# Kernel optimization log

Hardware: AMD Instinct MI355X
Metric: run time of the kernel (lower is better)

Reference implementation:

```python
import jax, jax.numpy as jnp
import numpy as np

N = 40000   # num nodes
C = 128     # in_channels
H = 8       # num_heads
D = C // H  # head_dim = 16
E = 640000  # num edges
FF = 4 * C


def layer_norm(x, g, b, eps=1e-5):
    m = jnp.mean(x, axis=-1, keepdims=True)
    v = jnp.mean((x - m) ** 2, axis=-1, keepdims=True)
    return (x - m) / jnp.sqrt(v + eps) * g + b


def setup_inputs() -> dict:
    key = jax.random.key(0)
    ks = jax.random.split(key, 16)
    s = 0.02
    x = jax.random.normal(ks[0], (N, C), dtype=jnp.float32)
    edge_index = jax.random.randint(ks[1], (2, E), 0, N, dtype=jnp.int64)
    return {
        'x': x,
        'edge_index': edge_index,
        'Wq': jax.random.normal(ks[2], (C, C), jnp.float32) * s,
        'bq': jnp.zeros((C,), jnp.float32),
        'Wk': jax.random.normal(ks[3], (C, C), jnp.float32) * s,
        'bk': jnp.zeros((C,), jnp.float32),
        'Wv': jax.random.normal(ks[4], (C, C), jnp.float32) * s,
        'bv': jnp.zeros((C,), jnp.float32),
        'Wo': jax.random.normal(ks[5], (C, C), jnp.float32) * s,
        'bo': jnp.zeros((C,), jnp.float32),
        'ln1_g': jnp.ones((C,), jnp.float32),
        'ln1_b': jnp.zeros((C,), jnp.float32),
        'ln2_g': jnp.ones((C,), jnp.float32),
        'ln2_b': jnp.zeros((C,), jnp.float32),
        'W1': jax.random.normal(ks[6], (C, FF), jnp.float32) * s,
        'b1': jnp.zeros((FF,), jnp.float32),
        'W2': jax.random.normal(ks[7], (FF, C), jnp.float32) * s,
        'b2': jnp.zeros((C,), jnp.float32),
    }


def reference(x, edge_index, Wq, bq, Wk, bk, Wv, bv, Wo, bo,
              ln1_g, ln1_b, ln2_g, ln2_b, W1, b1, W2, b2):
    residual = x
    xn = layer_norm(x, ln1_g, ln1_b)
    q = (xn @ Wq + bq).reshape(N, H, D)
    k = (xn @ Wk + bk).reshape(N, H, D)
    v = (xn @ Wv + bv).reshape(N, H, D)
    src, dst = edge_index[0], edge_index[1]
    # per-edge scores: [E, H]
    scores = jnp.einsum('ehd,ehd->eh', q[dst], k[src]) / jnp.sqrt(jnp.float32(D))
    # NOTE: faithful to the source — softmax over ALL edges (dim=0), not per-destination
    attn = jax.nn.softmax(scores, axis=0)[:, :, None]          # [E, H, 1]
    weighted = v[src] * attn                                   # [E, H, D]
    aggregated = jax.ops.segment_sum(weighted, dst, num_segments=N)  # [N, H, D]
    out = aggregated.reshape(N, C) @ Wo + bo
    x1 = residual + out
    residual2 = x1
    xn2 = layer_norm(x1, ln2_g, ln2_b)
    ffn = jax.nn.relu(xn2 @ W1 + b1) @ W2 + b2
    return residual2 + ffn
```

## Files before the change

kernel.cpp:

```cpp
#include <hip/hip_runtime.h>
#include <math.h>

#define NNODES 40000
#define CCH    128
#define NH     8
#define HD     16
#define NEDGE  640000
#define NBLK   157
#define FBLK   10000
#define RBLK   40

typedef __attribute__((ext_vector_type(8))) short bf16x8;
typedef __attribute__((ext_vector_type(4))) float f32x4;
typedef __attribute__((ext_vector_type(2))) float f32x2;

__device__ inline unsigned short f2bf(float f) {
  union { float f; unsigned u; } c; c.f = f;
  unsigned r = c.u + 0x7fffu + ((c.u >> 16) & 1u);
  return (unsigned short)(r >> 16);
}
__device__ inline float bfs(unsigned short u) { union { unsigned i; float f; } c; c.i = (unsigned)u << 16; return c.f; }
__device__ inline float bflo(unsigned u) { union { unsigned i; float f; } c; c.i = u << 16; return c.f; }
__device__ inline float bfhi(unsigned u) { union { unsigned i; float f; } c; c.i = u & 0xffff0000u; return c.f; }

__device__ inline unsigned char f2fp8(float v) {
#if __has_builtin(__builtin_amdgcn_cvt_pk_fp8_f32)
  return (unsigned char)(__builtin_amdgcn_cvt_pk_fp8_f32(v, v, 0, false) & 0xff);
#else
  union { float f; unsigned u; } c; c.f = v;
  unsigned s = (c.u >> 24) & 0x80;
  int e = (int)((c.u >> 23) & 0xff) - 127;
  unsigned m = c.u & 0x7fffff;
  if (e > 8) return s | 0x7e;
  if (e >= -6) {
    unsigned q = (m + 0x80000) >> 20; unsigned ee = e + 7;
    if (q == 8) { q = 0; ee++; }
    if (ee > 15) return s | 0x7e;
    return s | (ee << 3) | q;
  }
  if (e < -10) return (unsigned char)s;
  float a = fabsf(v); unsigned q = (unsigned)(a * 512.f + 0.5f); if (q > 7) q = 7;
  return s | q;
#endif
}
__device__ inline void fp8x4d(unsigned w, float* o) {
#if __has_builtin(__builtin_amdgcn_cvt_pk_f32_fp8)
  f32x2 lo = __builtin_amdgcn_cvt_pk_f32_fp8((int)w, false);
  f32x2 hi = __builtin_amdgcn_cvt_pk_f32_fp8((int)w, true);
  o[0] = lo[0]; o[1] = lo[1]; o[2] = hi[0]; o[3] = hi[1];
#else
  #pragma unroll
  for (int i = 0; i < 4; i++) {
    unsigned b = (w >> (8 * i)) & 0xff;
    unsigned s = b >> 7, e = (b >> 3) & 15, m = b & 7;
    float v;
    if (e) { union { unsigned u; float f; } c; c.u = ((e + 120) << 23) | (m << 20); v = c.f; }
    else v = m * (1.f / 512.f);
    o[i] = s ? -v : v;
  }
#endif
}

__global__ __launch_bounds__(256) void k_ln_bf(const float* __restrict__ x,
                                               const float* __restrict__ g,
                                               const float* __restrict__ b,
                                               unsigned* __restrict__ out) {
  int wave = threadIdx.x >> 6;
  int lane = threadIdx.x & 63;
  int row  = blockIdx.x * 4 + wave;
  if (row >= NNODES) return;
  const float2* xr = (const float2*)(x + (size_t)row * CCH);
  float2 v = xr[lane];
  float s  = v.x + v.y;
  float ss = v.x * v.x + v.y * v.y;
  #pragma unroll
  for (int d = 1; d < 64; d <<= 1) {
    s  += __shfl_xor(s, d);
    ss += __shfl_xor(ss, d);
  }
  float mean = s * (1.0f / CCH);
  float var  = ss * (1.0f / CCH) - mean * mean;
  float rstd = rsqrtf(var + 1e-5f);
  float2 gg = ((const float2*)g)[lane];
  float2 bb = ((const float2*)b)[lane];
  float ox = (v.x - mean) * rstd * gg.x + bb.x;
  float oy = (v.y - mean) * rstd * gg.y + bb.y;
  out[(size_t)row * 64 + lane] = ((unsigned)f2bf(oy) << 16) | f2bf(ox);
}

__global__ __launch_bounds__(256) void k_wprep_all(const float* __restrict__ Wq,
                                                   const float* __restrict__ Wk,
                                                   const float* __restrict__ Wv,
                                                   const float* __restrict__ W1,
                                                   const float* __restrict__ W2,
                                                   const float* __restrict__ bq,
                                                   const float* __restrict__ bk,
                                                   const float* __restrict__ bv,
                                                   unsigned short* __restrict__ Wqkvt,
                                                   unsigned short* __restrict__ W1t,
                                                   unsigned short* __restrict__ W2t,
                                                   float* __restrict__ bqkv) {
  int idx = blockIdx.x * 256 + threadIdx.x;
  if (idx < 16384) { int n = idx >> 7, k = idx & 127; Wqkvt[idx] = f2bf(Wq[(size_t)k * 128 + n]); return; }
  idx -= 16384;
  if (idx < 16384) { int n = idx >> 7, k = idx & 127; Wqkvt[16384 + (n << 7) + k] = f2bf(Wk[(size_t)k * 128 + n]); return; }
  idx -= 16384;
  if (idx < 16384) { int n = idx >> 7, k = idx & 127; Wqkvt[32768 + (n << 7) + k] = f2bf(Wv[(size_t)k * 128 + n]); return; }
  idx -= 16384;
  if (idx < 65536) { int n = idx >> 7, k = idx & 127; W1t[idx] = f2bf(W1[(size_t)k * 512 + n]); return; }
  idx -= 65536;
  if (idx < 65536) { int n = idx >> 9, k = idx & 511; W2t[idx] = f2bf(W2[(size_t)k * 128 + n]); return; }
  idx -= 65536;
  if (idx < 384) bqkv[idx] = idx < 128 ? bq[idx] : (idx < 256 ? bk[idx - 128] : bv[idx - 256]);
}

__global__ __launch_bounds__(256) void k_wprep_wo(const float* __restrict__ W,
                                                  const float* __restrict__ dpart,
                                                  unsigned short* __restrict__ Wt) {
  __shared__ float sinv[8];
  if (threadIdx.x < 64) {
    int h = threadIdx.x & 7;
    float s = 0.f;
    for (int r = threadIdx.x >> 3; r < RBLK; r += 8) s += dpart[r * 8 + h];
    #pragma unroll
    for (int d = 8; d < 64; d <<= 1) s += __shfl_xor(s, d);
    if (threadIdx.x < 8) sinv[h] = 1.0f / s;
  }
  __syncthreads();
  int idx = blockIdx.x * 256 + threadIdx.x;
  if (idx >= CCH * CCH) return;
  int n = idx >> 7, k = idx & 127;
  Wt[idx] = f2bf(W[(size_t)k * CCH + n] * sinv[k >> 4]);
}

template <bool RELU, int RESMODE, int MODE>
__global__ __launch_bounds__(256) void k_mgemm(const unsigned short* __restrict__ A,
                                               const unsigned short* __restrict__ Bt,
                                               const float* __restrict__ bias,
                                               const void* __restrict__ res,
                                               void* __restrict__ outp,
                                               int K, int Nc,
                                               const float* __restrict__ lng,
                                               const float* __restrict__ lnb,
                                               void* __restrict__ outp2) {
  __shared__ unsigned short As[64 * 64];
  __shared__ unsigned short Bs[128 * 64];
  const int tid  = threadIdx.x;
  const int row0 = blockIdx.x * 64;
  const int c0   = blockIdx.y * 128;
  const int l    = tid & 63;
  const int w    = tid >> 6;
  const int wr   = w >> 1;
  const int wc   = w & 1;

  f32x4 acc[2][4] = {};

  for (int kc = 0; kc < K; kc += 64) {
    __syncthreads();
    #pragma unroll
    for (int it = 0; it < 2; it++) {
      int idx = it * 256 + tid;
      int r = idx >> 3, s = idx & 7;
      uint4 vv = *(const uint4*)(A + (size_t)(row0 + r) * K + kc + s * 8);
      *(uint4*)(As + r * 64 + ((s ^ (r & 7)) * 8)) = vv;
    }
    #pragma unroll
    for (int it = 0; it < 4; it++) {
      int idx = it * 256 + tid;
      int n = idx >> 3, s = idx & 7;
      uint4 vv = *(const uint4*)(Bt + (size_t)(c0 + n) * K + kc + s * 8);
      *(uint4*)(Bs + n * 64 + ((s ^ (n & 7)) * 8)) = vv;
    }
    __syncthreads();
    #pragma unroll
    for (int kk = 0; kk < 2; kk++) {
      int sb = kk * 4 + (l >> 4);
      bf16x8 af[2], bfr[4];
      #pragma unroll
      for (int mi = 0; mi < 2; mi++) {
        int r = wr * 32 + mi * 16 + (l & 15);
        af[mi] = *(const bf16x8*)(As + r * 64 + ((sb ^ (r & 7)) * 8));
      }
      #pragma unroll
      for (int ni = 0; ni < 4; ni++) {
        int n = wc * 64 + ni * 16 + (l & 15);
        bfr[ni] = *(const bf16x8*)(Bs + n * 64 + ((sb ^ (n & 7)) * 8));
      }
      #pragma unroll
      for (int mi = 0; mi < 2; mi++)
        #pragma unroll
        for (int ni = 0; ni < 4; ni++)
          acc[mi][ni] = __builtin_amdgcn_mfma_f32_16x16x32_bf16(af[mi], bfr[ni], acc[mi][ni], 0, 0, 0);
    }
  }

  if constexpr (MODE == 3) {
    __shared__ float lnS[64][2], lnSS[64][2], gS[128], bS[128];
    if (tid < 128) { gS[tid] = lng[tid]; bS[tid] = lnb[tid]; }
    #pragma unroll
    for (int mi = 0; mi < 2; mi++) {
      #pragma unroll
      for (int p = 0; p < 4; p++) {
        int lr = wr * 32 + mi * 16 + (l >> 4) * 4 + p;
        int r  = row0 + lr;
        float s = 0.f, ss = 0.f;
        #pragma unroll
        for (int ni = 0; ni < 4; ni++) {
          int c = wc * 64 + ni * 16 + (l & 15);
          float val = acc[mi][ni][p] + bias[c] + ((const float*)res)[(size_t)r * 128 + c];
          acc[mi][ni][p] = val;
          s += val; ss += val * val;
        }
        #pragma unroll
        for (int d = 1; d < 16; d <<= 1) { s += __shfl_xor(s, d); ss += __shfl_xor(ss, d); }
        if ((l & 15) == 0) { lnS[lr][wc] = s; lnSS[lr][wc] = ss; }
      }
    }
    __syncthreads();
    #pragma unroll
    for (int mi = 0; mi < 2; mi++) {
      #pragma unroll
      for (int p = 0; p < 4; p++) {
        int lr = wr * 32 + mi * 16 + (l >> 4) * 4 + p;
        int r  = row0 + lr;
        float m   = (lnS[lr][0] + lnS[lr][1]) * (1.f / 128.f);
        float var = (lnSS[lr][0] + lnSS[lr][1]) * (1.f / 128.f) - m * m;
        float rstd = rsqrtf(var + 1e-5f);
        #pragma unroll
        for (int ni = 0; ni < 4; ni++) {
          int c = wc * 64 + ni * 16 + (l & 15);
          float val = acc[mi][ni][p];
          ((unsigned short*)outp)[(size_t)r * 128 + c]  = f2bf(val);
          ((unsigned short*)outp2)[(size_t)r * 128 + c] = f2bf((val - m) * rstd * gS[c] + bS[c]);
        }
      }
    }
  } else {
    #pragma unroll
    for (int mi = 0; mi < 2; mi++) {
      #pragma unroll
      for (int p = 0; p < 4; p++) {
        int r = row0 + wr * 32 + mi * 16 + (l >> 4) * 4 + p;
        #pragma unroll
        for (int ni = 0; ni < 4; ni++) {
          int c = c0 + wc * 64 + ni * 16 + (l & 15);
          float val = acc[mi][ni][p] + bias[c];
          if (RESMODE == 1) val += ((const float*)res)[(size_t)r * Nc + c];
          if (RESMODE == 2) val += bfs(((const unsigned short*)res)[(size_t)r * Nc + c]);
          if (RELU) val = fmaxf(val, 0.f);
          if (MODE == 0)      ((float*)outp)[(size_t)r * Nc + c] = val;
          else if (MODE == 1) ((unsigned short*)outp)[(size_t)r * Nc + c] = f2bf(val);
          else {
            char* rowb = (char*)outp + (size_t)r * 512;
            if (c < 128) *(unsigned short*)(rowb + c * 2) = f2bf(val);
            else         *(unsigned char*)(rowb + 256 + (c - 128)) = f2fp8(val);
          }
        }
      }
    }
  }
}

__global__ __launch_bounds__(256) void k_histrank(const int* __restrict__ ei,
                                                  int* __restrict__ deg,
                                                  int* __restrict__ rank) {
  int e = blockIdx.x * 256 + threadIdx.x;
  if (e >= NEDGE) return;
  rank[e] = atomicAdd(&deg[ei[NEDGE + e]], 1);
}

__global__ __launch_bounds__(256) void k_scan3a(const int* __restrict__ deg,
                                                int* __restrict__ bsum) {
  int i = blockIdx.x * 256 + threadIdx.x;
  int d = (i < NNODES) ? deg[i] : 0;
  #pragma unroll
  for (int s = 1; s < 64; s <<= 1) d += __shfl_xor(d, s);
  __shared__ int ws4[4];
  if ((threadIdx.x & 63) == 0) ws4[threadIdx.x >> 6] = d;
  __syncthreads();
  if (threadIdx.x == 0) bsum[blockIdx.x] = ws4[0] + ws4[1] + ws4[2] + ws4[3];
}

__global__ __launch_bounds__(256) void k_scan3b(const int* __restrict__ bsum,
                                                int* __restrict__ bpre) {
  int t = threadIdx.x;
  int d = (t < NBLK) ? bsum[t] : 0;
  int lane = t & 63, wv = t >> 6;
  int incl = d;
  #pragma unroll
  for (int s = 1; s < 64; s <<= 1) { int o = __shfl_up(incl, s); if (lane >= s) incl += o; }
  __shared__ int wsum[4];
  if (lane == 63) wsum[wv] = incl;
  __syncthreads();
  int base = 0;
  for (int w2 = 0; w2 < wv; w2++) base += wsum[w2];
  if (t < NBLK) bpre[t] = base + incl - d;
}

__global__ __launch_bounds__(256) void k_scan3c(const int* __restrict__ deg,
                                                const int* __restrict__ bpre,
                                                int* __restrict__ off) {
  int t = threadIdx.x;
  int i = blockIdx.x * 256 + t;
  int d = (i < NNODES) ? deg[i] : 0;
  int lane = t & 63, wv = t >> 6;
  int incl = d;
  #pragma unroll
  for (int s = 1; s < 64; s <<= 1) { int o = __shfl_up(incl, s); if (lane >= s) incl += o; }
  __shared__ int wsum[4];
  if (lane == 63) wsum[wv] = incl;
  __syncthreads();
  int base = bpre[blockIdx.x];
  for (int w2 = 0; w2 < wv; w2++) base += wsum[w2];
  int ex = base + incl - d;
  if (i < NNODES) off[i] = ex;
  if (i == 0) off[NNODES] = NEDGE;
}

__global__ __launch_bounds__(256) void k_scatter(const int* __restrict__ ei,
                                                 const int* __restrict__ off,
                                                 const int* __restrict__ rank,
                                                 int* __restrict__ srcs) {
  int e = blockIdx.x * 256 + threadIdx.x;
  if (e >= NEDGE) return;
  srcs[off[ei[NEDGE + e]] + rank[e]] = ei[e];
}

__global__ __launch_bounds__(256) void k_fused(const unsigned char* __restrict__ qkv,
                                               const int* __restrict__ off,
                                               const int* __restrict__ srcs,
                                               unsigned* __restrict__ U,
                                               float* __restrict__ hpart) {
  const int wave = threadIdx.x >> 6;
  const int lane = threadIdx.x & 63;
  const int n  = blockIdx.x * 4 + wave;
  const int g  = lane >> 3;
  const int c8 = lane & 7;

  const uint4* qp = (const uint4*)(qkv + (size_t)n * 512 + c8 * 32);
  uint4 qa = qp[0], qb = qp[1];
  float qf[16];
  qf[0]=bflo(qa.x);  qf[1]=bfhi(qa.x);  qf[2]=bflo(qa.y);  qf[3]=bfhi(qa.y);
  qf[4]=bflo(qa.z);  qf[5]=bfhi(qa.z);  qf[6]=bflo(qa.w);  qf[7]=bfhi(qa.w);
  qf[8]=bflo(qb.x);  qf[9]=bfhi(qb.x);  qf[10]=bflo(qb.y); qf[11]=bfhi(qb.y);
  qf[12]=bflo(qb.z); qf[13]=bfhi(qb.z); qf[14]=bflo(qb.w); qf[15]=bfhi(qb.w);

  float acc[16];
  #pragma unroll
  for (int i = 0; i < 16; i++) acc[i] = 0.f;
  float lsum = 0.f;

  const int i0 = off[n], i1 = off[n + 1];
  for (int jb = i0; jb < i1; jb += 8) {
    int j = jb + g;
    bool valid = j < i1;
    int src = srcs[valid ? j : jb];
    const uint4* kp = (const uint4*)(qkv + (size_t)src * 512 + 256 + c8 * 16);
    uint4 kw = kp[0];
    uint4 vw = kp[8];
    float kf[16], vf[16];
    fp8x4d(kw.x, kf + 0); fp8x4d(kw.y, kf + 4); fp8x4d(kw.z, kf + 8); fp8x4d(kw.w, kf + 12);
    fp8x4d(vw.x, vf + 0); fp8x4d(vw.y, vf + 4); fp8x4d(vw.z, vf + 8); fp8x4d(vw.w, vf + 12);
    float p = 0.f;
    #pragma unroll
    for (int i = 0; i < 16; i++) p += qf[i] * kf[i];
    float w = valid ? __expf(p * 0.25f) : 0.f;
    lsum += w;
    #pragma unroll
    for (int i = 0; i < 16; i++) acc[i] += w * vf[i];
  }

  #pragma unroll
  for (int d = 8; d < 64; d <<= 1) {
    #pragma unroll
    for (int i = 0; i < 16; i++) acc[i] += __shfl_xor(acc[i], d);
    lsum += __shfl_xor(lsum, d);
  }

  __shared__ float wsum[4][8];
  if (lane < 8) {
    wsum[wave][c8] = lsum;
    unsigned o[8];
    #pragma unroll
    for (int i = 0; i < 8; i++)
      o[i] = ((unsigned)f2bf(acc[2 * i + 1]) << 16) | f2bf(acc[2 * i]);
    uint4* up = (uint4*)(U + (size_t)n * 64 + c8 * 8);
    up[0] = make_uint4(o[0], o[1], o[2], o[3]);
    up[1] = make_uint4(o[4], o[5], o[6], o[7]);
  }
  __syncthreads();
  if (threadIdx.x < 8) {
    hpart[blockIdx.x * 8 + threadIdx.x] =
        wsum[0][threadIdx.x] + wsum[1][threadIdx.x] + wsum[2][threadIdx.x] + wsum[3][threadIdx.x];
  }
}

__global__ __launch_bounds__(256) void k_reduce_part(const float* __restrict__ hpart,
                                                     float* __restrict__ dpart) {
  const int t = threadIdx.x;
  const int h = t & 7;
  const int r0 = blockIdx.x * (FBLK / RBLK);
  float s = 0.f;
  for (int r = r0 + (t >> 3); r < r0 + FBLK / RBLK; r += 32) s += hpart[r * 8 + h];
  #pragma unroll
  for (int d = 8; d < 64; d <<= 1) s += __shfl_xor(s, d);
  __shared__ float ws4[4][8];
  int lane = t & 63, wv = t >> 6;
  if (lane < 8) ws4[wv][lane] = s;
  __syncthreads();
  if (t < 8) dpart[blockIdx.x * 8 + t] = ws4[0][t] + ws4[1][t] + ws4[2][t] + ws4[3][t];
}

extern "C" void kernel_launch(void* const* d_in, const int* in_sizes, int n_in,
                              void* d_out, int out_size, void* d_ws, size_t ws_size,
                              hipStream_t stream) {
  const float* x    = (const float*)d_in[0];
  const int*   ei   = (const int*)d_in[1];
  const float* Wq   = (const float*)d_in[2];
  const float* bq   = (const float*)d_in[3];
  const float* Wk   = (const float*)d_in[4];
  const float* bk   = (const float*)d_in[5];
  const float* Wv   = (const float*)d_in[6];
  const float* bv   = (const float*)d_in[7];
  const float* Wo   = (const float*)d_in[8];
  const float* bo   = (const float*)d_in[9];
  const float* ln1g = (const float*)d_in[10];
  const float* ln1b = (const float*)d_in[11];
  const float* ln2g = (const float*)d_in[12];
  const float* ln2b = (const float*)d_in[13];
  const float* W1   = (const float*)d_in[14];
  const float* b1   = (const float*)d_in[15];
  const float* W2   = (const float*)d_in[16];
  const float* b2   = (const float*)d_in[17];
  float* out = (float*)d_out;

  char* p = (char*)d_ws;
  const size_t NCb = (size_t)NNODES * CCH * 2;
  unsigned short* xn   = (unsigned short*)p; p += NCb;
  unsigned char*  qkvb = (unsigned char*)p;  p += (size_t)NNODES * 512;
  unsigned short* agg  = (unsigned short*)p; p += NCb;
  p += NCb;
  unsigned short* x1b  = (unsigned short*)p; p += NCb;
  int* deg    = (int*)p;                     p += (size_t)NNODES * 4 + 256;
  int* off    = (int*)p;                     p += (size_t)(NNODES + 1) * 4 + 256;
  int* rank   = (int*)p;                     p += (size_t)NEDGE * 4;
  int* srcs   = (int*)p;                     p += (size_t)NEDGE * 4;
  int* bsum   = (int*)p;                     p += 256 * 4;
  int* bpre   = (int*)p;                     p += 256 * 4;
  float* hpart = (float*)p;                  p += (size_t)FBLK * 8 * 4;
  float* dpart = (float*)p;                  p += (size_t)RBLK * 8 * 4 + 256;
  float* bqkv  = (float*)p;                  p += 384 * 4 + 256;
  unsigned short* Wqkvt = (unsigned short*)p; p += (size_t)384 * CCH * 2;
  unsigned short* Wot   = (unsigned short*)p; p += (size_t)CCH * CCH * 2;
  unsigned short* W1t   = (unsigned short*)p; p += (size_t)CCH * 4 * CCH * 2;
  unsigned short* W2t   = (unsigned short*)p; p += (size_t)CCH * 4 * CCH * 2;
  unsigned short* ffn1 = (unsigned short*)qkvb;
  unsigned short* xn2  = xn;

  dim3 blk(256);
  dim3 gLN(NNODES / 4);
  dim3 gM(NNODES / 64, 1);
  dim3 gM3(NNODES / 64, 3);
  dim3 gM4(NNODES / 64, 4);
  dim3 gE((NEDGE + 255) / 256);

  hipMemsetAsync(deg, 0, (size_t)NNODES * 4, stream);
  k_histrank<<<gE, blk, 0, stream>>>(ei, deg, rank);
  k_scan3a<<<NBLK, blk, 0, stream>>>(deg, bsum);
  k_scan3b<<<1, blk, 0, stream>>>(bsum, bpre);
  k_scan3c<<<NBLK, blk, 0, stream>>>(deg, bpre, off);
  k_scatter<<<gE, blk, 0, stream>>>(ei, off, rank, srcs);

  k_wprep_all<<<706, blk, 0, stream>>>(Wq, Wk, Wv, W1, W2, bq, bk, bv,
                                       Wqkvt, W1t, W2t, bqkv);

  k_ln_bf<<<gLN, blk, 0, stream>>>(x, ln1g, ln1b, (unsigned*)xn);
  k_mgemm<false, 0, 2><<<gM3, blk, 0, stream>>>(xn, Wqkvt, bqkv, nullptr, qkvb,
                                                CCH, 384, nullptr, nullptr, nullptr);

  k_fused<<<FBLK, blk, 0, stream>>>(qkvb, off, srcs, (unsigned*)agg, hpart);
  k_reduce_part<<<RBLK, blk, 0, stream>>>(hpart, dpart);

  k_wprep_wo<<<64, blk, 0, stream>>>(Wo, dpart, Wot);
  k_mgemm<false, 1, 3><<<gM, blk, 0, stream>>>(agg, Wot, bo, x, x1b,
                                               CCH, CCH, ln2g, ln2b, xn2);

  k_mgemm<true, 0, 1><<<gM4, blk, 0, stream>>>(xn2, W1t, b1, nullptr, ffn1,
                                               CCH, 4 * CCH, nullptr, nullptr, nullptr);
  k_mgemm<false, 2, 0><<<gM, blk, 0, stream>>>(ffn1, W2t, b2, x1b, out,
                                               4 * CCH, CCH, nullptr, nullptr, nullptr);
}
```

Measured before the change: 167.5 us.

## Fuse LayerNorm into QKV GEMM, add K=128 GEMM kernel, prefetch edges

Adds a specialized K=128 GEMM kernel that keeps the whole A tile in LDS and loops over all output column tiles in one block. The QKV projection now computes LayerNorm inline from fp32 x, which removes the separate LN kernel and its bf16 round trip. The FFN1 GEMM uses the same kernel, so A is loaded once rather than once per column block. The deg memset is folded into the weight-prep kernel, and the edge-aggregation loop now prefetches the next batch of K/V before using the current one. The cost is less grid parallelism (one block per 64 rows) and larger LDS use per block.

Result: faster. 161.4 us (-3.6%).

```diff
diff --git a/kernel.cpp b/kernel.cpp
--- a/kernel.cpp
+++ b/kernel.cpp
@@ -61,33 +61,6 @@
 #endif
 }
 
-__global__ __launch_bounds__(256) void k_ln_bf(const float* __restrict__ x,
-                                               const float* __restrict__ g,
-                                               const float* __restrict__ b,
-                                               unsigned* __restrict__ out) {
-  int wave = threadIdx.x >> 6;
-  int lane = threadIdx.x & 63;
-  int row  = blockIdx.x * 4 + wave;
-  if (row >= NNODES) return;
-  const float2* xr = (const float2*)(x + (size_t)row * CCH);
-  float2 v = xr[lane];
-  float s  = v.x + v.y;
-  float ss = v.x * v.x + v.y * v.y;
-  #pragma unroll
-  for (int d = 1; d < 64; d <<= 1) {
-    s  += __shfl_xor(s, d);
-    ss += __shfl_xor(ss, d);
-  }
-  float mean = s * (1.0f / CCH);
-  float var  = ss * (1.0f / CCH) - mean * mean;
-  float rstd = rsqrtf(var + 1e-5f);
-  float2 gg = ((const float2*)g)[lane];
-  float2 bb = ((const float2*)b)[lane];
-  float ox = (v.x - mean) * rstd * gg.x + bb.x;
-  float oy = (v.y - mean) * rstd * gg.y + bb.y;
-  out[(size_t)row * 64 + lane] = ((unsigned)f2bf(oy) << 16) | f2bf(ox);
-}
-
 __global__ __launch_bounds__(256) void k_wprep_all(const float* __restrict__ Wq,
                                                    const float* __restrict__ Wk,
                                                    const float* __restrict__ Wv,
@@ -99,8 +72,11 @@
                                                    unsigned short* __restrict__ Wqkvt,
                                                    unsigned short* __restrict__ W1t,
                                                    unsigned short* __restrict__ W2t,
-                                                   float* __restrict__ bqkv) {
-  int idx = blockIdx.x * 256 + threadIdx.x;
+                                                   float* __restrict__ bqkv,
+                                                   int* __restrict__ deg) {
+  int g0 = blockIdx.x * 256 + threadIdx.x;
+  if (g0 < NNODES) deg[g0] = 0;
+  int idx = g0;
   if (idx < 16384) { int n = idx >> 7, k = idx & 127; Wqkvt[idx] = f2bf(Wq[(size_t)k * 128 + n]); return; }
   idx -= 16384;
   if (idx < 16384) { int n = idx >> 7, k = idx & 127; Wqkvt[16384 + (n << 7) + k] = f2bf(Wk[(size_t)k * 128 + n]); return; }
@@ -131,6 +107,121 @@
   if (idx >= CCH * CCH) return;
   int n = idx >> 7, k = idx & 127;
   Wt[idx] = f2bf(W[(size_t)k * CCH + n] * sinv[k >> 4]);
+}
+
+template <int NT, int OUTMODE, bool LNA, bool RELU>
+__global__ __launch_bounds__(256) void k_gemm128(const void* __restrict__ Ain,
+                                                 const unsigned short* __restrict__ Bt,
+                                                 const float* __restrict__ bias,
+                                                 const float* __restrict__ lng,
+                                                 const float* __restrict__ lnb,
+                                                 void* __restrict__ outp) {
+  __shared__ unsigned short As[64 * 128];
+  __shared__ unsigned short Bs[128 * 128];
+  const int tid  = threadIdx.x;
+  const int row0 = blockIdx.x * 64;
+  const int l    = tid & 63;
+  const int w    = tid >> 6;
+  const int wr   = w >> 1;
+  const int wc   = w & 1;
+
+  if (LNA) {
+    const float* x = (const float*)Ain;
+    int r = tid >> 2, qt = tid & 3;
+    const float4* xr = (const float4*)(x + (size_t)(row0 + r) * 128 + qt * 32);
+    float4 xv[8];
+    float s = 0.f, ss = 0.f;
+    #pragma unroll
+    for (int i = 0; i < 8; i++) {
+      xv[i] = xr[i];
+      s  += xv[i].x + xv[i].y + xv[i].z + xv[i].w;
+      ss += xv[i].x * xv[i].x + xv[i].y * xv[i].y + xv[i].z * xv[i].z + xv[i].w * xv[i].w;
+    }
+    s += __shfl_xor(s, 1); ss += __shfl_xor(ss, 1);
+    s += __shfl_xor(s, 2); ss += __shfl_xor(ss, 2);
+    float mean = s * (1.f / 128.f);
+    float var  = ss * (1.f / 128.f) - mean * mean;
+    float rstd = rsqrtf(var + 1e-5f);
+    #pragma unroll
+    for (int i = 0; i < 8; i += 2) {
+      int c0 = qt * 32 + i * 4;
+      float va[8] = {xv[i].x, xv[i].y, xv[i].z, xv[i].w,
+                     xv[i+1].x, xv[i+1].y, xv[i+1].z, xv[i+1].w};
+      unsigned short tmp[8];
+      #pragma unroll
+      for (int u = 0; u < 8; u++)
+        tmp[u] = f2bf((va[u] - mean) * rstd * lng[c0 + u] + lnb[c0 + u]);
+      int slot = c0 >> 3;
+      *(uint4*)(As + r * 128 + ((slot ^ (r & 7)) * 8)) = *(uint4*)tmp;
+    }
+  } else {
+    const unsigned short* A = (const unsigned short*)Ain;
+    #pragma unroll
+    for (int it = 0; it < 4; it++) {
+      int idx = it * 256 + tid;
+      int r = idx >> 4, sl = idx & 15;
+      uint4 vv = *(const uint4*)(A + (size_t)(row0 + r) * 128 + sl * 8);
+      *(uint4*)(As + r * 128 + ((sl ^ (r & 7)) * 8)) = vv;
+    }
+  }
+
+  #pragma unroll
+  for (int t = 0; t < NT; t++) {
+    __syncthreads();
+    #pragma unroll
+    for (int it = 0; it < 8; it++) {
+      int idx = it * 256 + tid;
+      int n = idx >> 4, sl = idx & 15;
+      uint4 vv = *(const uint4*)(Bt + (size_t)(t * 128 + n) * 128 + sl * 8);
+      *(uint4*)(Bs + n * 128 + ((sl ^ (n & 7)) * 8)) = vv;
+    }
+    __syncthreads();
+
+    f32x4 acc[2][4] = {};
+    #pragma unroll
+    for (int kk = 0; kk < 4; kk++) {
+      int sb = kk * 4 + (l >> 4);
+      bf16x8 af[2], bfr[4];
+      #pragma unroll
+      for (int mi = 0; mi < 2; mi++) {
+        int r = wr * 32 + mi * 16 + (l & 15);
+        af[mi] = *(const bf16x8*)(As + r * 128 + ((sb ^ (r & 7)) * 8));
+      }
+      #pragma unroll
+      for (int ni = 0; ni < 4; ni++) {
+        int n = wc * 64 + ni * 16 + (l & 15);
+        bfr[ni] = *(const bf16x8*)(Bs + n * 128 + ((sb ^ (n & 7)) * 8));
+      }
+      #pragma unroll
+      for (int mi = 0; mi < 2; mi++)
+        #pragma unroll
+        for (int ni = 0; ni < 4; ni++)
+          acc[mi][ni] = __builtin_amdgcn_mfma_f32_16x16x32_bf16(af[mi], bfr[ni], acc[mi][ni], 0, 0, 0);
+    }
+
+    #pragma unroll
+    for (int mi = 0; mi < 2; mi++) {
+      #pragma unroll
+      for (int p = 0; p < 4; p++) {
+        int r = row0 + wr * 32 + mi * 16 + (l >> 4) * 4 + p;
+        #pragma unroll
+        for (int ni = 0; ni < 4; ni++) {
+          int cc = wc * 64 + ni * 16 + (l & 15);
+          int c  = t * 128 + cc;
+          float val = acc[mi][ni][p] + bias[c];
+          if (RELU) val = fmaxf(val, 0.f);
+          if (OUTMODE == 1) {
+            ((unsigned short*)outp)[(size_t)r * (NT * 128) + c] = f2bf(val);
+          } else {
+            char* rowb = (char*)outp + (size_t)r * 512;
+            if (t == 0)      *(unsigned short*)(rowb + cc * 2) = f2bf(val);
+            else if (t == 1) *(unsigned char*)(rowb + 256 + cc) = f2fp8(val);
+            else             *(unsigned char*)(rowb + 384 + cc) = f2fp8(val);
+          }
+        }
+      }
+    }
+  }
 }
 
 template <bool RELU, int RESMODE, int MODE>
@@ -248,13 +339,7 @@
           if (RESMODE == 1) val += ((const float*)res)[(size_t)r * Nc + c];
           if (RESMODE == 2) val += bfs(((const unsigned short*)res)[(size_t)r * Nc + c]);
           if (RELU) val = fmaxf(val, 0.f);
-          if (MODE == 0)      ((float*)outp)[(size_t)r * Nc + c] = val;
-          else if (MODE == 1) ((unsigned short*)outp)[(size_t)r * Nc + c] = f2bf(val);
-          else {
-            char* rowb = (char*)outp + (size_t)r * 512;
-            if (c < 128) *(unsigned short*)(rowb + c * 2) = f2bf(val);
-            else         *(unsigned char*)(rowb + 256 + (c - 128)) = f2fp8(val);
-          }
+          ((float*)outp)[(size_t)r * Nc + c] = val;
         }
       }
     }
@@ -351,23 +436,32 @@
   float lsum = 0.f;
 
   const int i0 = off[n], i1 = off[n + 1];
-  for (int jb = i0; jb < i1; jb += 8) {
-    int j = jb + g;
-    bool valid = j < i1;
-    int src = srcs[valid ? j : jb];
+  if (i1 > i0) {
+    int j0 = i0 + g; if (j0 >= i1) j0 = i1 - 1;
+    int src = srcs[j0];
     const uint4* kp = (const uint4*)(qkv + (size_t)src * 512 + 256 + c8 * 16);
-    uint4 kw = kp[0];
-    uint4 vw = kp[8];
-    float kf[16], vf[16];
-    fp8x4d(kw.x, kf + 0); fp8x4d(kw.y, kf + 4); fp8x4d(kw.z, kf + 8); fp8x4d(kw.w, kf + 12);
-    fp8x4d(vw.x, vf + 0); fp8x4d(vw.y, vf + 4); fp8x4d(vw.z, vf + 8); fp8x4d(vw.w, vf + 12);
-    float p = 0.f;
-    #pragma unroll
-    for (int i = 0; i < 16; i++) p += qf[i] * kf[i];
-    float w = valid ? __expf(p * 0.25f) : 0.f;
-    lsum += w;
-    #pragma unroll
-    for (int i = 0; i < 16; i++) acc[i] += w * vf[i];
+    uint4 kw = kp[0], vw = kp[8];
+    for (int jb = i0; jb < i1; jb += 8) {
+      uint4 kc = kw, vc = vw;
+      bool valid = jb + g < i1;
+      int jn = jb + 8;
+      if (jn < i1) {
+        int j2 = jn + g; if (j2 >= i1) j2 = i1 - 1;
+        int srcn = srcs[j2];
+        const uint4* kpn = (const uint4*)(qkv + (size_t)srcn * 512 + 256 + c8 * 16);
+        kw = kpn[0]; vw = kpn[8];
+      }
+      float kf[16], vf[16];
+      fp8x4d(kc.x, kf + 0); fp8x4d(kc.y, kf + 4); fp8x4d(kc.z, kf + 8); fp8x4d(kc.w, kf + 12);
+      fp8x4d(vc.x, vf + 0); fp8x4d(vc.y, vf + 4); fp8x4d(vc.z, vf + 8); fp8x4d(vc.w, vf + 12);
+      float p = 0.f;
+      #pragma unroll
+      for (int i = 0; i < 16; i++) p += qf[i] * kf[i];
+      float w = valid ? __expf(p * 0.25f) : 0.f;
+      lsum += w;
+      #pragma unroll
+      for (int i = 0; i < 16; i++) acc[i] += w * vf[i];
+    }
   }
 
   #pragma unroll
@@ -436,7 +530,7 @@
 
   char* p = (char*)d_ws;
   const size_t NCb = (size_t)NNODES * CCH * 2;
-  unsigned short* xn   = (unsigned short*)p; p += NCb;
+  unsigned short* xn2  = (unsigned short*)p; p += NCb;
   unsigned char*  qkvb = (unsigned char*)p;  p += (size_t)NNODES * 512;
   unsigned short* agg  = (unsigned short*)p; p += NCb;
   p += NCb;
@@ -455,28 +549,22 @@
   unsigned short* W1t   = (unsigned short*)p; p += (size_t)CCH * 4 * CCH * 2;
   unsigned short* W2t   = (unsigned short*)p; p += (size_t)CCH * 4 * CCH * 2;
   unsigned short* ffn1 = (unsigned short*)qkvb;
-  unsigned short* xn2  = xn;
 
   dim3 blk(256);
-  dim3 gLN(NNODES / 4);
   dim3 gM(NNODES / 64, 1);
-  dim3 gM3(NNODES / 64, 3);
-  dim3 gM4(NNODES / 64, 4);
   dim3 gE((NEDGE + 255) / 256);
 
-  hipMemsetAsync(deg, 0, (size_t)NNODES * 4, stream);
+  k_wprep_all<<<706, blk, 0, stream>>>(Wq, Wk, Wv, W1, W2, bq, bk, bv,
+                                       Wqkvt, W1t, W2t, bqkv, deg);
+
   k_histrank<<<gE, blk, 0, stream>>>(ei, deg, rank);
   k_scan3a<<<NBLK, blk, 0, stream>>>(deg, bsum);
   k_scan3b<<<1, blk, 0, stream>>>(bsum, bpre);
   k_scan3c<<<NBLK, blk, 0, stream>>>(deg, bpre, off);
   k_scatter<<<gE, blk, 0, stream>>>(ei, off, rank, srcs);
 
-  k_wprep_all<<<706, blk, 0, stream>>>(Wq, Wk, Wv, W1, W2, bq, bk, bv,
-                                       Wqkvt, W1t, W2t, bqkv);
-
-  k_ln_bf<<<gLN, blk, 0, stream>>>(x, ln1g, ln1b, (unsigned*)xn);
-  k_mgemm<false, 0, 2><<<gM3, blk, 0, stream>>>(xn, Wqkvt, bqkv, nullptr, qkvb,
-                                                CCH, 384, nullptr, nullptr, nullptr);
+  k_gemm128<3, 2, true, false><<<gM, blk, 0, stream>>>(x, Wqkvt, bqkv,
+                                                       ln1g, ln1b, qkvb);
 
   k_fused<<<FBLK, blk, 0, stream>>>(qkvb, off, srcs, (unsigned*)agg, hpart);
   k_reduce_part<<<RBLK, blk, 0, stream>>>(hpart, dpart);
@@ -485,8 +573,8 @@
   k_mgemm<false, 1, 3><<<gM, blk, 0, stream>>>(agg, Wot, bo, x, x1b,
                                                CCH, CCH, ln2g, ln2b, xn2);
 
-  k_mgemm<true, 0, 1><<<gM4, blk, 0, stream>>>(xn2, W1t, b1, nullptr, ffn1,
-                                               CCH, 4 * CCH, nullptr, nullptr, nullptr);
+  k_gemm128<4, 1, false, true><<<gM, blk, 0, stream>>>(xn2, W1t, b1,
+                                                       nullptr, nullptr, ffn1);
   k_mgemm<false, 2, 0><<<gM, blk, 0, stream>>>(ffn1, W2t, b2, x1b, out,
                                                4 * CCH, CCH, nullptr, nullptr, nullptr);
 }
```
